# Optimization experiments

Hardware: AMD Instinct MI355X
Metric: run time of the kernel (lower is better)

The kernel has to match this reference:

```python
import jax, jax.numpy as jnp
import numpy as np

N_EXPERTS = 6
TOP_K = 2
IN_DIM, HID_DIM, OUT_DIM = 1024, 4096, 1024
N_TOKENS = 8192


def setup_inputs() -> dict:
    key = jax.random.key(0)
    ks = jax.random.split(key, 7)
    s_in = 1.0 / np.sqrt(IN_DIM)
    s_hid = 1.0 / np.sqrt(HID_DIM)
    return {
        "x": jax.random.normal(ks[0], (N_TOKENS, IN_DIM), dtype=jnp.float32),
        "Wg": jax.random.uniform(ks[1], (IN_DIM, N_EXPERTS), jnp.float32, -s_in, s_in),
        "bg": jax.random.uniform(ks[2], (N_EXPERTS,), jnp.float32, -s_in, s_in),
        "W1": jax.random.uniform(ks[3], (N_EXPERTS, IN_DIM, HID_DIM), jnp.float32, -s_in, s_in),
        "b1": jax.random.uniform(ks[4], (N_EXPERTS, HID_DIM), jnp.float32, -s_in, s_in),
        "W2": jax.random.uniform(ks[5], (N_EXPERTS, HID_DIM, OUT_DIM), jnp.float32, -s_hid, s_hid),
        "b2": jax.random.uniform(ks[6], (N_EXPERTS, OUT_DIM), jnp.float32, -s_hid, s_hid),
    }


def reference(x, Wg, bg, W1, b1, W2, b2):
    n_experts = Wg.shape[-1]
    # gating: scores [N, E]
    scores = x @ Wg + bg
    _, topk_idx = jax.lax.top_k(scores, TOP_K)  # [N, k]
    # binary mask of selected experts [N, E]
    mask = jax.nn.one_hot(topk_idx, n_experts, dtype=scores.dtype).sum(axis=1)
    weights = jax.nn.softmax(scores, axis=-1) * mask
    weights = weights / (weights.sum(axis=-1, keepdims=True) + 1e-8)
    # dense all-expert compute (faithful to original): hidden [N, E, H]
    h = jax.nn.relu(jnp.einsum("ni,eih->neh", x, W1) + b1)
    outputs = jnp.einsum("neh,eho->neo", h, W2) + b2  # [N, E, O]
    return jnp.einsum("ne,neo->no", weights, outputs)
```

## Files before the change

kernel.cpp:

```cpp
#include <hip/hip_runtime.h>

typedef unsigned short u16;
typedef float f32x4 __attribute__((ext_vector_type(4)));
typedef __bf16 bf16x8 __attribute__((ext_vector_type(8)));
typedef unsigned short u16x8 __attribute__((ext_vector_type(8)));
typedef unsigned short u16x4 __attribute__((ext_vector_type(4)));
typedef unsigned long long ull;

#define N_TOKENS 8192
#define IN_DIM   1024
#define HID_DIM  4096
#define OUT_DIM  1024
#define N_EXP    6

__device__ __forceinline__ u16 f2bf(float f) {
  union { float f; unsigned int u; } v; v.f = f;
  unsigned int u = v.u;
  unsigned int r = (u + 0x7FFFu + ((u >> 16) & 1u)) >> 16;
  return (u16)r;
}

__device__ __forceinline__ float bf2f(u16 v) {
  union { unsigned int u; float f; } x; x.u = ((unsigned int)v) << 16; return x.f;
}

__device__ __forceinline__ void load_lds16(const void* g, void* l) {
  __builtin_amdgcn_global_load_lds(
      (const __attribute__((address_space(1))) void*)g,
      (__attribute__((address_space(3))) void*)l, 16, 0, 0);
}

__global__ __launch_bounds__(256) void prep_kernel(const float* __restrict__ W1,
                                                   u16* __restrict__ W1T,
                                                   const float* __restrict__ x,
                                                   const float* __restrict__ Wg,
                                                   const float* __restrict__ bg,
                                                   u16* __restrict__ xb,
                                                   int* __restrict__ gate_e,
                                                   float* __restrict__ gate_w) {
  __shared__ u16 tile[64][72];
  const int bid = blockIdx.x;
  if (bid < 6144) {
    const int ex = bid >> 10, ti = bid & 1023;
    const float* src = W1 + (size_t)ex * IN_DIM * HID_DIM;
    u16* dst = W1T + (size_t)ex * IN_DIM * HID_DIM;
    const int tx = ti & 63, ty = ti >> 6;
    const int C = HID_DIM, R = IN_DIM;
    int c0 = tx * 64, r0 = ty * 64;
    int t = threadIdx.x;
    int cc = (t & 15) * 4, rb = t >> 4;
#pragma unroll
    for (int p = 0; p < 4; p++) {
      int r = p * 16 + rb;
      float4 v = *(const float4*)(src + (size_t)(r0 + r) * C + c0 + cc);
      tile[cc + 0][r] = f2bf(v.x);
      tile[cc + 1][r] = f2bf(v.y);
      tile[cc + 2][r] = f2bf(v.z);
      tile[cc + 3][r] = f2bf(v.w);
    }
    __syncthreads();
    int c = t >> 2, rp = (t & 3) * 16;
    u16* dp = dst + (size_t)(c0 + c) * R + r0 + rp;
    *(u16x8*)(dp)     = *(const u16x8*)&tile[c][rp];
    *(u16x8*)(dp + 8) = *(const u16x8*)&tile[c][rp + 8];
    return;
  }
  const int gb = bid - 6144;
  int lane = threadIdx.x & 63, wid = threadIdx.x >> 6;
  int tok = gb * 4 + wid;
  float acc[N_EXP] = {0.f, 0.f, 0.f, 0.f, 0.f, 0.f};
  const float4* xr = (const float4*)(x + (size_t)tok * IN_DIM);
  u16* xw = xb + (size_t)tok * IN_DIM;
#pragma unroll
  for (int g = 0; g < 4; g++) {
    float4 v = xr[lane + g * 64];
    int c0 = (lane + g * 64) * 4;
    u16x4 o; o[0] = f2bf(v.x); o[1] = f2bf(v.y); o[2] = f2bf(v.z); o[3] = f2bf(v.w);
    *(u16x4*)(xw + c0) = o;
#pragma unroll
    for (int c = 0; c < 4; c++) {
      float xv = (c == 0) ? v.x : (c == 1) ? v.y : (c == 2) ? v.z : v.w;
      const float* wr = Wg + (c0 + c) * N_EXP;
#pragma unroll
      for (int e = 0; e < N_EXP; e++) acc[e] += xv * wr[e];
    }
  }
#pragma unroll
  for (int e = 0; e < N_EXP; e++) {
    float a = acc[e];
#pragma unroll
    for (int off = 32; off > 0; off >>= 1) a += __shfl_xor(a, off, 64);
    acc[e] = a;
  }
  if (lane == 0) {
    float s[N_EXP];
#pragma unroll
    for (int e = 0; e < N_EXP; e++) s[e] = acc[e] + bg[e];
    float mx = s[0];
#pragma unroll
    for (int e = 1; e < N_EXP; e++) mx = fmaxf(mx, s[e]);
    float p[N_EXP], sum = 0.f;
#pragma unroll
    for (int e = 0; e < N_EXP; e++) { p[e] = expf(s[e] - mx); sum += p[e]; }
    int a = 0;
#pragma unroll
    for (int e = 1; e < N_EXP; e++) if (s[e] > s[a]) a = e;
    int b = (a == 0) ? 1 : 0;
#pragma unroll
    for (int e = 0; e < N_EXP; e++) if (e != a && s[e] > s[b]) b = e;
    float pa = p[a] / sum, pb = p[b] / sum;
    float den = pa + pb + 1e-8f;
    gate_e[2 * tok] = a; gate_e[2 * tok + 1] = b;
    gate_w[2 * tok] = pa / den; gate_w[2 * tok + 1] = pb / den;
  }
}

__global__ __launch_bounds__(384) void routing_kernel(const int* __restrict__ gate_e,
                                                      int* __restrict__ idxl,
                                                      int* __restrict__ tokslot,
                                                      int* __restrict__ meta) {
  int wave = threadIdx.x >> 6, lane = threadIdx.x & 63;
  __shared__ int s_cnt[N_EXP];
  if (wave < N_EXP) {
    const int e = wave;
    int cnt = 0;
    const int4* gp = (const int4*)gate_e;
    int4 g = gp[lane];
    const ull below = (1ull << lane) - 1ull;
    for (int it = 0; it < N_TOKENS / 128; it++) {
      int4 gn;
      if (it + 1 < N_TOKENS / 128) gn = gp[(it + 1) * 64 + lane];
      bool s0 = (g.x == e) || (g.y == e);
      bool s1 = (g.z == e) || (g.w == e);
      ull m0 = __ballot(s0), m1 = __ballot(s1);
      int p0 = __popcll(m0 & below) + __popcll(m1 & below);
      int t0 = it * 128 + 2 * lane;
      if (s0) {
        int j = cnt + p0;
        idxl[e * N_TOKENS + j] = t0;
        tokslot[2 * t0 + ((g.x == e) ? 0 : 1)] = j;
      }
      if (s1) {
        int j = cnt + p0 + (s0 ? 1 : 0);
        idxl[e * N_TOKENS + j] = t0 + 1;
        tokslot[2 * (t0 + 1) + ((g.z == e) ? 0 : 1)] = j;
      }
      cnt += __popcll(m0) + __popcll(m1);
      g = gn;
    }
    if (lane == 0) s_cnt[e] = cnt;
  }
  __syncthreads();
  if (threadIdx.x == 0) {
    int off = 0;
    for (int e = 0; e < N_EXP; e++) { meta[e] = s_cnt[e]; meta[8 + e] = off; off += s_cnt[e]; }
    meta[8 + N_EXP] = off;
  }
}


#define GDS_A(AH) \
  _Pragma("unroll") for (int mi = 0; mi < 4; mi++) { \
    int r_ = (AH)*128 + wr*64 + mi*16 + lrow; \
    af[mi][0] = *(const bf16x8*)&sA[cur][r_*64 + ((lhi ^ lx7) * 8)]; \
    af[mi][1] = *(const bf16x8*)&sA[cur][r_*64 + (((4 + lhi) ^ lx7) * 8)]; }

#define GDS_B(BH) \
  _Pragma("unroll") for (int nj = 0; nj < 2; nj++) { \
    int r_ = (BH)*128 + wc*32 + nj*16 + lrow; \
    bfr[nj][0] = *(const bf16x8*)&sB[cur][r_*64 + ((lhi ^ lx7) * 8)]; \
    bfr[nj][1] = *(const bf16x8*)&sB[cur][r_*64 + (((4 + lhi) ^ lx7) * 8)]; }

#define GSTG_A(HH) \
  load_lds16(pa[HH][0] + ksn, &sA[nxt][((HH)*128 + wave*16) * 64]); \
  load_lds16(pa[HH][1] + ksn, &sA[nxt][((HH)*128 + wave*16 + 8) * 64]);

#define GSTG_B(HH) \
  load_lds16(pb[HH][0] + ksn, &sB[nxt][((HH)*128 + wave*16) * 64]); \
  load_lds16(pb[HH][1] + ksn, &sB[nxt][((HH)*128 + wave*16 + 8) * 64]);

#define GMFMA_Q(AH, BH) \
  _Pragma("unroll") for (int mi = 0; mi < 4; mi++) \
  _Pragma("unroll") for (int nj = 0; nj < 2; nj++) { \
    acc[AH][BH][mi][nj] = __builtin_amdgcn_mfma_f32_16x16x32_bf16(af[mi][0], bfr[nj][0], acc[AH][BH][mi][nj], 0, 0, 0); \
    acc[AH][BH][mi][nj] = __builtin_amdgcn_mfma_f32_16x16x32_bf16(af[mi][1], bfr[nj][1], acc[AH][BH][mi][nj], 0, 0, 0); }

#define GBAR __builtin_amdgcn_s_barrier()
#define GLGKM0 asm volatile("s_waitcnt lgkmcnt(0)" ::: "memory")
#define GVMC(n) asm volatile("s_waitcnt vmcnt(" #n ")" ::: "memory")

#define GEMM_KLOOP(NT_)                                                        \
  { const int ksn = 0; const int nxt = 0;                                      \
    GSTG_A(0); GSTG_B(0); GSTG_A(1); GSTG_B(1); }                              \
  GVMC(4);                                                                     \
  GBAR;                                                                        \
  int cur = 0;                                                                 \
  for (int t = 0; t < (NT_); t++) {                                            \
    const int nxt = cur ^ 1;                                                   \
    const int ksn = ((t + 1 < (NT_)) ? (t + 1) : ((NT_) - 1)) * 64;            \
                                                          \
    GDS_A(0); GDS_B(0);                                                        \
    GSTG_A(0);                                                                 \
    GBAR; GLGKM0;                                                              \
    __builtin_amdgcn_s_setprio(1); GMFMA_Q(0, 0); __builtin_amdgcn_s_setprio(0); \
    GVMC(2); GBAR;                                                             \
                                                          \
    GDS_B(1);                                                                  \
    GSTG_B(0);                                                                 \
    GBAR; GLGKM0;                                                              \
    __builtin_amdgcn_s_setprio(1); GMFMA_Q(0, 1); __builtin_amdgcn_s_setprio(0); \
    GBAR;                                                                      \
                                                          \
    GDS_A(1); GDS_B(0);                                                        \
    GSTG_A(1);                                                                 \
    GBAR; GLGKM0;                                                              \
    __builtin_amdgcn_s_setprio(1); GMFMA_Q(1, 0); __builtin_amdgcn_s_setprio(0); \
    GBAR;                                                                      \
                                                          \
    GDS_B(1);                                                                  \
    GSTG_B(1);                                                                 \
    GBAR; GLGKM0;                                                              \
    __builtin_amdgcn_s_setprio(1); GMFMA_Q(1, 1); __builtin_amdgcn_s_setprio(0); \
    GVMC(4); GBAR;                                                             \
    cur = nxt;                                                                 \
  }

__device__ __forceinline__ void decode_expert(const int* meta, int mtg,
                                              int& e, int& mt, int& cnt) {
  e = -1; mt = 0; cnt = 0;
  int sum = 0;
#pragma unroll
  for (int ee = 0; ee < N_EXP; ee++) {
    int c = meta[ee];
    int nt = (c + 255) >> 8;
    if (e < 0 && mtg < sum + nt) { e = ee; mt = mtg - sum; cnt = c; }
    sum += nt;
  }
}

__global__ __launch_bounds__(512) void gemm1_kernel(const u16* __restrict__ xb,
                                                    const u16* __restrict__ W1T,
                                                    const float* __restrict__ b1,
                                                    const int* __restrict__ idxl,
                                                    const int* __restrict__ meta,
                                                    u16* __restrict__ h,
                                                    const float* __restrict__ W2,
                                                    u16* __restrict__ W2T) {
  __shared__ u16 sA[2][16384];
  __shared__ u16 sB[2][16384];
  const int bid = blockIdx.x;
  if (bid >= 1152) {
    u16 (*tile)[72] = (u16(*)[72])&sA[0][0];
    const int ti = bid - 1152;
    const int ex = ti >> 10;
    const int t2 = ti & 1023;
    const int tx = t2 & 15, ty = t2 >> 4;
    const float* src = W2 + (size_t)ex * HID_DIM * OUT_DIM;
    u16* dst = W2T + (size_t)ex * HID_DIM * OUT_DIM;
    const int C = OUT_DIM, R = HID_DIM;
    const int c0 = tx * 64, r0 = ty * 64;
    const int t = threadIdx.x;
    const int cc = (t & 15) * 4, rb = t >> 4;
#pragma unroll
    for (int p = 0; p < 2; p++) {
      int r = p * 32 + rb;
      float4 v = *(const float4*)(src + (size_t)(r0 + r) * C + c0 + cc);
      tile[cc + 0][r] = f2bf(v.x);
      tile[cc + 1][r] = f2bf(v.y);
      tile[cc + 2][r] = f2bf(v.z);
      tile[cc + 3][r] = f2bf(v.w);
    }
    __syncthreads();
    const int c = t >> 3, rp = (t & 7) * 8;
    *(u16x8*)(dst + (size_t)(c0 + c) * R + r0 + rp) = *(const u16x8*)&tile[c][rp];
    return;
  }
  const int xcd = bid & 7;
  const int s = bid >> 3;
  const int chunk = s / 36, q = s % 36;
  const int n = chunk * 4 + (q & 3);
  const int mtg = xcd * 9 + (q >> 2);

  int e, mt, cnt;
  decode_expert(meta, mtg, e, mt, cnt);
  if (e < 0) return;
  const int off = meta[8 + e];
  const int bn0 = n * 256;
  const int tid = threadIdx.x, lane = tid & 63, wave = tid >> 6;
  const int wr = wave >> 2, wc = wave & 3;
  const int lrow = lane & 15, lhi = lane >> 4, lx7 = lane & 7;
  const int schunk = (lane & 7) ^ (lane >> 3);

  const u16* pa[2][2];
  const u16* pb[2][2];
  const u16* bbase = W1T + (size_t)e * HID_DIM * IN_DIM;
#pragma unroll
  for (int hh = 0; hh < 2; hh++)
#pragma unroll
    for (int i = 0; i < 2; i++) {
      int gr = hh * 128 + wave * 16 + i * 8 + (lane >> 3);
      int j = mt * 256 + gr; if (j >= cnt) j = cnt - 1;
      int tok = idxl[e * N_TOKENS + j];
      pa[hh][i] = xb + (size_t)tok * IN_DIM + schunk * 8;
      pb[hh][i] = bbase + (size_t)(bn0 + gr) * IN_DIM + schunk * 8;
    }

  f32x4 acc[2][2][4][2] = {};
  bf16x8 af[4][2], bfr[2][2];

  GEMM_KLOOP(IN_DIM / 64)

#pragma unroll
  for (int ah = 0; ah < 2; ah++)
#pragma unroll
    for (int bh = 0; bh < 2; bh++)
#pragma unroll
      for (int nj = 0; nj < 2; nj++) {
        int col = bn0 + bh * 128 + wc * 32 + nj * 16 + lrow;
        float bias = b1[e * HID_DIM + col];
#pragma unroll
        for (int mi = 0; mi < 4; mi++)
#pragma unroll
          for (int rr = 0; rr < 4; rr++) {
            int j = mt * 256 + ah * 128 + wr * 64 + mi * 16 + lhi * 4 + rr;
            if (j < cnt) {
              float v = fmaxf(acc[ah][bh][mi][nj][rr] + bias, 0.f);
              h[(size_t)(off + j) * HID_DIM + col] = f2bf(v);
            }
          }
      }
}

__global__ __launch_bounds__(512) void gemm2_kernel(const u16* __restrict__ hbuf,
                                                    const u16* __restrict__ W2T,
                                                    const float* __restrict__ b2,
                                                    const int* __restrict__ meta,
                                                    u16* __restrict__ y0,
                                                    u16* __restrict__ y1) {
  __shared__ u16 sA[2][16384];
  __shared__ u16 sB[2][16384];
  const int bid = blockIdx.x;
  const int xcd = bid & 7;
  const int s = bid >> 3;
  const int v = s & 7;
  const int mtg = xcd * 9 + (s >> 3);
  const int n = v >> 1, kzid = v & 1;

  int e, mt, cnt;
  decode_expert(meta, mtg, e, mt, cnt);
  if (e < 0) return;
  const int off = meta[8 + e];
  const int bn0 = n * 256;
  const int kz = kzid * (HID_DIM / 2);
  const int tid = threadIdx.x, lane = tid & 63, wave = tid >> 6;
  const int wr = wave >> 2, wc = wave & 3;
  const int lrow = lane & 15, lhi = lane >> 4, lx7 = lane & 7;
  const int schunk = (lane & 7) ^ (lane >> 3);

  const u16* pa[2][2];
  const u16* pb[2][2];
  const u16* bbase = W2T + (size_t)e * OUT_DIM * HID_DIM;
#pragma unroll
  for (int hh = 0; hh < 2; hh++)
#pragma unroll
    for (int i = 0; i < 2; i++) {
      int gr = hh * 128 + wave * 16 + i * 8 + (lane >> 3);
      int j = mt * 256 + gr; if (j >= cnt) j = cnt - 1;
      pa[hh][i] = hbuf + (size_t)(off + j) * HID_DIM + kz + schunk * 8;
      pb[hh][i] = bbase + (size_t)(bn0 + gr) * HID_DIM + kz + schunk * 8;
    }

  f32x4 acc[2][2][4][2] = {};
  bf16x8 af[4][2], bfr[2][2];

  GEMM_KLOOP(HID_DIM / 2 / 64)

  u16* __restrict__ yb = kzid ? y1 : y0;
#pragma unroll
  for (int ah = 0; ah < 2; ah++)
#pragma unroll
    for (int bh = 0; bh < 2; bh++)
#pragma unroll
      for (int nj = 0; nj < 2; nj++) {
        int col = bn0 + bh * 128 + wc * 32 + nj * 16 + lrow;
        float bias = (kzid == 0) ? b2[e * OUT_DIM + col] : 0.f;
#pragma unroll
        for (int mi = 0; mi < 4; mi++)
#pragma unroll
          for (int rr = 0; rr < 4; rr++) {
            int j = mt * 256 + ah * 128 + wr * 64 + mi * 16 + lhi * 4 + rr;
            if (j < cnt)
              yb[(size_t)(off + j) * OUT_DIM + col] = f2bf(acc[ah][bh][mi][nj][rr] + bias);
          }
      }
}

__global__ __launch_bounds__(256) void combine_kernel(const u16* __restrict__ y0,
                                                      const u16* __restrict__ y1,
                                                      const int* __restrict__ gate_e,
                                                      const float* __restrict__ gate_w,
                                                      const int* __restrict__ tokslot,
                                                      const int* __restrict__ meta,
                                                      float* __restrict__ out) {
  const int t = blockIdx.x;
  const int e0 = gate_e[2 * t], e1 = gate_e[2 * t + 1];
  const float w0 = gate_w[2 * t], w1 = gate_w[2 * t + 1];
  const size_t s0 = (size_t)(meta[8 + e0] + tokslot[2 * t]) * OUT_DIM;
  const size_t s1 = (size_t)(meta[8 + e1] + tokslot[2 * t + 1]) * OUT_DIM;
  const int c = threadIdx.x * 4;
  u16x4 a0 = *(const u16x4*)(y0 + s0 + c);
  u16x4 b0 = *(const u16x4*)(y1 + s0 + c);
  u16x4 a1 = *(const u16x4*)(y0 + s1 + c);
  u16x4 b1 = *(const u16x4*)(y1 + s1 + c);
  float4 o;
  o.x = w0 * (bf2f(a0[0]) + bf2f(b0[0])) + w1 * (bf2f(a1[0]) + bf2f(b1[0]));
  o.y = w0 * (bf2f(a0[1]) + bf2f(b0[1])) + w1 * (bf2f(a1[1]) + bf2f(b1[1]));
  o.z = w0 * (bf2f(a0[2]) + bf2f(b0[2])) + w1 * (bf2f(a1[2]) + bf2f(b1[2]));
  o.w = w0 * (bf2f(a0[3]) + bf2f(b0[3])) + w1 * (bf2f(a1[3]) + bf2f(b1[3]));
  *(float4*)(out + (size_t)t * OUT_DIM + c) = o;
}

extern "C" void kernel_launch(void* const* d_in, const int* in_sizes, int n_in,
                              void* d_out, int out_size, void* d_ws, size_t ws_size,
                              hipStream_t stream) {
  const float* x  = (const float*)d_in[0];
  const float* Wg = (const float*)d_in[1];
  const float* bg = (const float*)d_in[2];
  const float* W1 = (const float*)d_in[3];
  const float* b1 = (const float*)d_in[4];
  const float* W2 = (const float*)d_in[5];
  const float* b2 = (const float*)d_in[6];
  float* out = (float*)d_out;

  char* ws = (char*)d_ws;
  u16*   xb     = (u16*)(ws);
  u16*   W1T    = (u16*)(ws + 16777216);
  u16*   y0     = (u16*)(ws);
  u16*   y1     = (u16*)(ws + 33554432);
  u16*   W2T    = (u16*)(ws + 67108864);
  u16*   h      = (u16*)(ws + 117440512);
  int*   gate_e = (int*)(ws + 251658240);
  float* gate_w = (float*)(ws + 251723776);
  int*   idxl   = (int*)(ws + 251789312);
  int*   tokslot= (int*)(ws + 251985920);
  int*   meta   = (int*)(ws + 252051456);

  prep_kernel<<<8192, 256, 0, stream>>>(W1, W1T, x, Wg, bg, xb, gate_e, gate_w);
  routing_kernel<<<1, 384, 0, stream>>>(gate_e, idxl, tokslot, meta);
  gemm1_kernel<<<7296, 512, 0, stream>>>(xb, W1T, b1, idxl, meta, h, W2, W2T);
  gemm2_kernel<<<576, 512, 0, stream>>>(h, W2T, b2, meta, y0, y1);
  combine_kernel<<<N_TOKENS, 256, 0, stream>>>(y0, y1, gate_e, gate_w, tokslot, meta, out);
}
```

Baseline: 532.9 us.

## Deepen GEMM K-loop prefetch to stage tiles two iterations ahead

Restructures the double-buffered GEMM main loop so global-to-LDS loads for A and B quarter-tiles are issued up to two K-steps ahead. Each one goes into a buffer region as soon as its last reader has finished, instead of loading only the next tile. The prologue now preloads most of two stages, and the vmcnt waits are relaxed from 4 to 6, allowing more loads in flight. This aims to hide global memory latency better behind MFMA work. The cost is trickier buffer-reuse ordering, which relies on barriers to avoid overwriting data still being read.

New measurement: 637.7 us. 19.7% more time.

```diff
diff --git a/kernel.cpp b/kernel.cpp
--- a/kernel.cpp
+++ b/kernel.cpp
@@ -171,13 +171,13 @@
     bfr[nj][0] = *(const bf16x8*)&sB[cur][r_*64 + ((lhi ^ lx7) * 8)]; \
     bfr[nj][1] = *(const bf16x8*)&sB[cur][r_*64 + (((4 + lhi) ^ lx7) * 8)]; }
 
-#define GSTG_A(HH) \
-  load_lds16(pa[HH][0] + ksn, &sA[nxt][((HH)*128 + wave*16) * 64]); \
-  load_lds16(pa[HH][1] + ksn, &sA[nxt][((HH)*128 + wave*16 + 8) * 64]);
-
-#define GSTG_B(HH) \
-  load_lds16(pb[HH][0] + ksn, &sB[nxt][((HH)*128 + wave*16) * 64]); \
-  load_lds16(pb[HH][1] + ksn, &sB[nxt][((HH)*128 + wave*16 + 8) * 64]);
+#define STG_A(BUF, HH, KS) \
+  load_lds16(pa[HH][0] + (KS), &sA[BUF][((HH)*128 + wave*16) * 64]); \
+  load_lds16(pa[HH][1] + (KS), &sA[BUF][((HH)*128 + wave*16 + 8) * 64]);
+
+#define STG_B(BUF, HH, KS) \
+  load_lds16(pb[HH][0] + (KS), &sB[BUF][((HH)*128 + wave*16) * 64]); \
+  load_lds16(pb[HH][1] + (KS), &sB[BUF][((HH)*128 + wave*16 + 8) * 64]);
 
 #define GMFMA_Q(AH, BH) \
   _Pragma("unroll") for (int mi = 0; mi < 4; mi++) \
@@ -188,41 +188,41 @@
 #define GBAR __builtin_amdgcn_s_barrier()
 #define GLGKM0 asm volatile("s_waitcnt lgkmcnt(0)" ::: "memory")
 #define GVMC(n) asm volatile("s_waitcnt vmcnt(" #n ")" ::: "memory")
+#define GPRIO1 __builtin_amdgcn_s_setprio(1)
+#define GPRIO0 __builtin_amdgcn_s_setprio(0)
 
 #define GEMM_KLOOP(NT_)                                                        \
-  { const int ksn = 0; const int nxt = 0;                                      \
-    GSTG_A(0); GSTG_B(0); GSTG_A(1); GSTG_B(1); }                              \
-  GVMC(4);                                                                     \
+  { STG_A(0, 0, 0) STG_B(0, 0, 0) STG_A(0, 1, 0) STG_B(0, 1, 0)                \
+    STG_A(1, 0, 64) STG_B(1, 0, 64) STG_A(1, 1, 64) }                          \
+  GVMC(6);                                                                     \
   GBAR;                                                                        \
-  int cur = 0;                                                                 \
   for (int t = 0; t < (NT_); t++) {                                            \
-    const int nxt = cur ^ 1;                                                   \
-    const int ksn = ((t + 1 < (NT_)) ? (t + 1) : ((NT_) - 1)) * 64;            \
-                                                          \
+    const int cur = t & 1, nxt = cur ^ 1;                                      \
+    const int kB1 = ((t + 1 < (NT_)) ? (t + 1) : ((NT_) - 1)) * 64;            \
+    const int k2  = ((t + 2 < (NT_)) ? (t + 2) : ((NT_) - 1)) * 64;            \
+                              \
     GDS_A(0); GDS_B(0);                                                        \
-    GSTG_A(0);                                                                 \
+    STG_B(nxt, 1, kB1)                                                         \
     GBAR; GLGKM0;                                                              \
-    __builtin_amdgcn_s_setprio(1); GMFMA_Q(0, 0); __builtin_amdgcn_s_setprio(0); \
-    GVMC(2); GBAR;                                                             \
-                                                          \
+    GPRIO1; GMFMA_Q(0, 0); GPRIO0;                                             \
+    GBAR;                                                                      \
+       \
     GDS_B(1);                                                                  \
-    GSTG_B(0);                                                                 \
+    STG_A(cur, 0, k2)                                                          \
     GBAR; GLGKM0;                                                              \
-    __builtin_amdgcn_s_setprio(1); GMFMA_Q(0, 1); __builtin_amdgcn_s_setprio(0); \
+    GPRIO1; GMFMA_Q(0, 1); GPRIO0;                                             \
     GBAR;                                                                      \
-                                                          \
+                        \
     GDS_A(1); GDS_B(0);                                                        \
-    GSTG_A(1);                                                                 \
     GBAR; GLGKM0;                                                              \
-    __builtin_amdgcn_s_setprio(1); GMFMA_Q(1, 0); __builtin_amdgcn_s_setprio(0); \
+    GPRIO1; GMFMA_Q(1, 0); GPRIO0;                                             \
     GBAR;                                                                      \
-                                                          \
+       \
     GDS_B(1);                                                                  \
-    GSTG_B(1);                                                                 \
+    STG_B(cur, 0, k2) STG_A(cur, 1, k2)                                        \
     GBAR; GLGKM0;                                                              \
-    __builtin_amdgcn_s_setprio(1); GMFMA_Q(1, 1); __builtin_amdgcn_s_setprio(0); \
-    GVMC(4); GBAR;                                                             \
-    cur = nxt;                                                                 \
+    GPRIO1; GMFMA_Q(1, 1); GPRIO0;                                             \
+    GVMC(6); GBAR;                                                             \
   }
 
 __device__ __forceinline__ void decode_expert(const int* meta, int mtg,
```
